# Kernel tuning notes

Measured on AMD Instinct MI355X. Metric: run time of the kernel, lower is better.

The kernel has to match this reference:

```python
import jax, jax.numpy as jnp
import numpy as np

MASK_ID = 3
MAX_SEN = 128
SEN_DIM = 128
EMBED = 1024


def setup_inputs() -> dict:
    key = jax.random.key(0)
    ks = jax.random.split(key, 12)
    B, S, E, D = 8, 8192, EMBED, SEN_DIM
    s = 0.02
    return {
        "input_ids": jax.random.randint(ks[0], (B, S), 0, 64),
        "hidden_states": jax.random.normal(ks[1], (B, S, E), jnp.float32),
        "Wv": jax.random.normal(ks[2], (E, D), jnp.float32) * s,
        "bv": jnp.zeros((D,), jnp.float32),
        "Wq": jax.random.normal(ks[3], (E, D), jnp.float32) * s,
        "bq": jnp.zeros((D,), jnp.float32),
        "Wk": jax.random.normal(ks[4], (D, D), jnp.float32) * s,
        "bk": jnp.zeros((D,), jnp.float32),
        "Wvt": jax.random.normal(ks[5], (D, D), jnp.float32) * s,
        "bvt": jnp.zeros((D,), jnp.float32),
        "Wo": jax.random.normal(ks[6], (D, E), jnp.float32) * s,
        "bo": jnp.zeros((E,), jnp.float32),
    }


def reference(input_ids, hidden_states, Wv, bv, Wq, bq, Wk, bk, Wvt, bvt, Wo, bo):
    B, S, E = hidden_states.shape
    dt = hidden_states.dtype

    # sentence segmentation: each mask token t with running count c belongs to bucket c-1
    mask = input_ids == MASK_ID                               # (B, S)
    csum = jnp.cumsum(mask.astype(jnp.int32), axis=1)         # (B, S)
    # tokens that are not mask tokens (or overflow max_sen_num) go to dummy bucket MAX_SEN
    seg = jnp.where(mask & (csum <= MAX_SEN), csum - 1, MAX_SEN)  # (B, S)

    # segment-sum replacement for torch.bmm(sen_pos_mask, hidden_states)
    b_idx = jnp.arange(B)[:, None]
    pooled = jnp.zeros((B, MAX_SEN + 1, E), dt).at[b_idx, seg].add(hidden_states)[:, :MAX_SEN]  # (B, M, E)

    static_sen_states = pooled @ Wv + bv                      # (B, M, 128)

    q_token = (hidden_states @ Wq + bq) * (SEN_DIM ** -0.5)   # (B, S, 128)
    k_sen = static_sen_states @ Wk + bk                       # (B, M, 128)
    v_sen = static_sen_states @ Wvt + bvt                     # (B, M, 128)

    # token t may attend to sentences 0..csum[t]-1
    tmp_mask = (jnp.arange(MAX_SEN)[None, None, :] + 1) <= csum[:, :, None]  # (B, S, M)
    neg = jnp.finfo(dt).min
    logits = jnp.einsum('bsd,bmd->bsm', q_token, k_sen) + jnp.where(tmp_mask, jnp.zeros((), dt), neg)
    attn = jax.nn.softmax(logits, axis=-1) * tmp_mask.astype(dt)  # (B, S, M)

    sen_attn_output = jnp.einsum('bsm,bmd->bsd', attn, v_sen) @ Wo + bo  # (B, S, E)
    return sen_attn_output
```

## Files before the change

kernel.cpp:

```cpp
#include <hip/hip_runtime.h>
#include <hip/hip_bf16.h>

#define MASK_ID 3
#define MAX_SEN 128
#define NB 8
#define SEQ 8192
#define EMB 1024
#define DIM 128
#define TS 32

typedef __attribute__((ext_vector_type(8))) short short8v;
typedef __attribute__((ext_vector_type(4))) float f32x4;

#define MFMA(a, b, c) __builtin_amdgcn_mfma_f32_16x16x32_bf16(a, b, c, 0, 0, 0)

__device__ __forceinline__ short f2b(float x) {
    union { float f; unsigned u; } v; v.f = x;
    unsigned r = (v.u + 0x7FFFu + ((v.u >> 16) & 1u)) >> 16;
    return (short)r;
}

__global__ __launch_bounds__(1024) void seg_kernel(const int* __restrict__ ids,
                                                   int* __restrict__ pos,
                                                   int* __restrict__ nvis) {
    int b = blockIdx.x;
    int tid = threadIdx.x;
    __shared__ int sc[1024];
    __shared__ int sc2[1024];
    const int PER = SEQ / 1024;
    int base = b * SEQ + tid * PER;

    int ids_l[PER];
    int cnt = 0;
    #pragma unroll
    for (int j = 0; j < PER; j++) {
        ids_l[j] = ids[base + j];
        cnt += (ids_l[j] == MASK_ID) ? 1 : 0;
    }
    if (tid < MAX_SEN) pos[b * MAX_SEN + tid] = -1;
    sc[tid] = cnt;
    __syncthreads();

    int* src = sc;
    int* dst = sc2;
    for (int off = 1; off < 1024; off <<= 1) {
        int v = src[tid];
        if (tid >= off) v += src[tid - off];
        dst[tid] = v;
        __syncthreads();
        int* t = src; src = dst; dst = t;
    }
    int incl = src[tid];
    int run = incl - cnt;

    #pragma unroll
    for (int j = 0; j < PER; j++) {
        if (ids_l[j] == MASK_ID) {
            run++;
            if (run <= MAX_SEN) pos[b * MAX_SEN + run - 1] = tid * PER + j;
        }
        int nv = run; if (nv > MAX_SEN) nv = MAX_SEN;
        nvis[base + j] = nv;
    }
}

__global__ __launch_bounds__(256) void prep_w(const float* __restrict__ Wq,
                                              const float* __restrict__ Wo,
                                              short* __restrict__ WqT,
                                              short* __restrict__ WoT) {
    int idx = blockIdx.x * 256 + threadIdx.x;
    int d = idx >> 10, e = idx & 1023;
    WqT[idx] = f2b(Wq[e * DIM + d]);
    int e2 = idx >> 7, d2 = idx & 127;
    WoT[idx] = f2b(Wo[d2 * EMB + e2]);
}

__global__ __launch_bounds__(128) void static_kernel(const float* __restrict__ hidden,
                                                     const float* __restrict__ Wv,
                                                     const float* __restrict__ bv,
                                                     const int* __restrict__ pos,
                                                     float* __restrict__ stat) {
    int m = blockIdx.x, b = blockIdx.y;
    int d = threadIdx.x;
    __shared__ float h[EMB];
    int p = pos[b * MAX_SEN + m];
    float acc = bv[d];
    if (p >= 0) {
        const float* hp = hidden + ((size_t)b * SEQ + p) * EMB;
        for (int e = d; e < EMB; e += 128) h[e] = hp[e];
        __syncthreads();
        for (int e = 0; e < EMB; e++) acc += h[e] * Wv[e * DIM + d];
    }
    stat[(b * MAX_SEN + m) * DIM + d] = acc;
}

__global__ __launch_bounds__(128) void kv_kernel(const float* __restrict__ stat,
                                                 const float* __restrict__ Wk, const float* __restrict__ bk,
                                                 const float* __restrict__ Wvt, const float* __restrict__ bvt,
                                                 short* __restrict__ k_bf, short* __restrict__ vT_bf) {
    int m = blockIdx.x, b = blockIdx.y;
    int d = threadIdx.x;
    __shared__ float srow[DIM];
    srow[d] = stat[(b * MAX_SEN + m) * DIM + d];
    __syncthreads();
    float ka = bk[d], va = bvt[d];
    for (int e = 0; e < DIM; e++) {
        float sv = srow[e];
        ka += sv * Wk[e * DIM + d];
        va += sv * Wvt[e * DIM + d];
    }
    k_bf[((size_t)b * MAX_SEN + m) * DIM + d] = f2b(ka);
    vT_bf[((size_t)b * DIM + d) * MAX_SEN + m] = f2b(va);
}

__global__ __launch_bounds__(256, 2) void attn_kernel(
    const float* __restrict__ hidden,
    const short* __restrict__ WqT, const float* __restrict__ bq,
    const short* __restrict__ k_bf, const short* __restrict__ vT_bf,
    const short* __restrict__ WoT, const float* __restrict__ bo,
    const int* __restrict__ nvis,
    float* __restrict__ out) {
    int blk = blockIdx.x;
    int b  = blk >> 8;
    int s0 = (blk & 255) * TS;
    int tid = threadIdx.x;
    int lane = tid & 63;
    int w  = tid >> 6;
    int lr = lane & 15;
    int lq = lane >> 4;

    __shared__ short hA[32 * 256];
    __shared__ short qP[32 * 128];
    __shared__ short odB[32 * 128];
    __shared__ float lg[32 * 132];

    char* hAc = (char*)hA;
    char* qPc = (char*)qP;
    char* odc = (char*)odB;

    const size_t hrow = (size_t)b * SEQ + s0;
    f32x4 zero = {0.f, 0.f, 0.f, 0.f};

    f32x4 a00 = zero, a01 = zero, a10 = zero, a11 = zero;
    for (int ec = 0; ec < 4; ec++) {
        __syncthreads();
        #pragma unroll
        for (int g = 0; g < 4; g++) {
            int G = tid + g * 256;
            int t = G >> 5;
            int e8 = (G & 31) << 3;
            const float* hp = hidden + (hrow + t) * EMB + ec * 256 + e8;
            float4 f0 = *(const float4*)hp;
            float4 f1 = *(const float4*)(hp + 4);
            short8v hh;
            hh[0] = f2b(f0.x); hh[1] = f2b(f0.y); hh[2] = f2b(f0.z); hh[3] = f2b(f0.w);
            hh[4] = f2b(f1.x); hh[5] = f2b(f1.y); hh[6] = f2b(f1.z); hh[7] = f2b(f1.w);
            int byte = (t * 512 + e8 * 2) ^ ((t & 7) << 4);
            *(short8v*)(hAc + byte) = hh;
        }
        __syncthreads();
        const short* bp0 = WqT + (w * 32 + lr) * 1024 + ec * 256 + lq * 8;
        const short* bp1 = bp0 + 16 * 1024;
        #pragma unroll
        for (int kk = 0; kk < 8; kk++) {
            short8v fa0 = *(short8v*)(hAc + ((lr * 512 + kk * 64 + lq * 16) ^ ((lr & 7) << 4)));
            short8v fa1 = *(short8v*)(hAc + (((16 + lr) * 512 + kk * 64 + lq * 16) ^ ((lr & 7) << 4)));
            short8v fb0 = *(const short8v*)(bp0 + kk * 32);
            short8v fb1 = *(const short8v*)(bp1 + kk * 32);
            a00 = MFMA(fa0, fb0, a00); a01 = MFMA(fa0, fb1, a01);
            a10 = MFMA(fa1, fb0, a10); a11 = MFMA(fa1, fb1, a11);
        }
    }
    {
        const float scale = 0.08838834764831845f;
        int d0 = w * 32 + lr;
        float bq0 = bq[d0], bq1 = bq[d0 + 16];
        #pragma unroll
        for (int r = 0; r < 4; r++) {
            int r0 = lq * 4 + r, r1 = 16 + r0;
            *(short*)(qPc + ((r0 * 256 + d0 * 2) ^ ((r0 & 7) << 4)))        = f2b((a00[r] + bq0) * scale);
            *(short*)(qPc + ((r0 * 256 + (d0 + 16) * 2) ^ ((r0 & 7) << 4))) = f2b((a01[r] + bq1) * scale);
            *(short*)(qPc + ((r1 * 256 + d0 * 2) ^ ((r1 & 7) << 4)))        = f2b((a10[r] + bq0) * scale);
            *(short*)(qPc + ((r1 * 256 + (d0 + 16) * 2) ^ ((r1 & 7) << 4))) = f2b((a11[r] + bq1) * scale);
        }
    }
    __syncthreads();

    {
        f32x4 l00 = zero, l01 = zero, l10 = zero, l11 = zero;
        const short* kbp0 = k_bf + ((size_t)b << 14) + (w * 32 + lr) * 128 + lq * 8;
        const short* kbp1 = kbp0 + 16 * 128;
        #pragma unroll
        for (int kk = 0; kk < 4; kk++) {
            short8v fa0 = *(short8v*)(qPc + ((lr * 256 + kk * 64 + lq * 16) ^ ((lr & 7) << 4)));
            short8v fa1 = *(short8v*)(qPc + (((16 + lr) * 256 + kk * 64 + lq * 16) ^ ((lr & 7) << 4)));
            short8v fb0 = *(const short8v*)(kbp0 + kk * 32);
            short8v fb1 = *(const short8v*)(kbp1 + kk * 32);
            l00 = MFMA(fa0, fb0, l00); l01 = MFMA(fa0, fb1, l01);
            l10 = MFMA(fa1, fb0, l10); l11 = MFMA(fa1, fb1, l11);
        }
        int m0 = w * 32 + lr;
        #pragma unroll
        for (int r = 0; r < 4; r++) {
            int r0 = lq * 4 + r, r1 = 16 + r0;
            lg[r0 * 132 + m0]      = l00[r];
            lg[r0 * 132 + m0 + 16] = l01[r];
            lg[r1 * 132 + m0]      = l10[r];
            lg[r1 * 132 + m0 + 16] = l11[r];
        }
    }
    __syncthreads();

    {
        int t = tid >> 3, sub = tid & 7;
        int nv = nvis[b * SEQ + s0 + t];
        float pv[16];
        float mx = -3.0e38f;
        #pragma unroll
        for (int i = 0; i < 16; i++) {
            int m = sub * 16 + i;
            float vv = lg[t * 132 + m];
            pv[i] = vv;
            if (m < nv) mx = fmaxf(mx, vv);
        }
        mx = fmaxf(mx, __shfl_xor(mx, 1));
        mx = fmaxf(mx, __shfl_xor(mx, 2));
        mx = fmaxf(mx, __shfl_xor(mx, 4));
        float sum = 0.f;
        #pragma unroll
        for (int i = 0; i < 16; i++) {
            int m = sub * 16 + i;
            float e = (m < nv) ? __expf(pv[i] - mx) : 0.f;
            pv[i] = e;
            sum += e;
        }
        sum += __shfl_xor(sum, 1);
        sum += __shfl_xor(sum, 2);
        sum += __shfl_xor(sum, 4);
        float inv = (nv > 0) ? 1.0f / sum : 0.f;
        #pragma unroll
        for (int i = 0; i < 16; i++) {
            int m = sub * 16 + i;
            *(short*)(qPc + ((t * 256 + m * 2) ^ ((t & 7) << 4))) = f2b(pv[i] * inv);
        }
    }
    __syncthreads();

    {
        f32x4 o00 = zero, o01 = zero, o10 = zero, o11 = zero;
        const short* vbp0 = vT_bf + ((size_t)b << 14) + (w * 32 + lr) * 128 + lq * 8;
        const short* vbp1 = vbp0 + 16 * 128;
        #pragma unroll
        for (int kk = 0; kk < 4; kk++) {
            short8v fa0 = *(short8v*)(qPc + ((lr * 256 + kk * 64 + lq * 16) ^ ((lr & 7) << 4)));
            short8v fa1 = *(short8v*)(qPc + (((16 + lr) * 256 + kk * 64 + lq * 16) ^ ((lr & 7) << 4)));
            short8v fb0 = *(const short8v*)(vbp0 + kk * 32);
            short8v fb1 = *(const short8v*)(vbp1 + kk * 32);
            o00 = MFMA(fa0, fb0, o00); o01 = MFMA(fa0, fb1, o01);
            o10 = MFMA(fa1, fb0, o10); o11 = MFMA(fa1, fb1, o11);
        }
        int d0 = w * 32 + lr;
        #pragma unroll
        for (int r = 0; r < 4; r++) {
            int r0 = lq * 4 + r, r1 = 16 + r0;
            *(short*)(odc + ((r0 * 256 + d0 * 2) ^ ((r0 & 7) << 4)))        = f2b(o00[r]);
            *(short*)(odc + ((r0 * 256 + (d0 + 16) * 2) ^ ((r0 & 7) << 4))) = f2b(o01[r]);
            *(short*)(odc + ((r1 * 256 + d0 * 2) ^ ((r1 & 7) << 4)))        = f2b(o10[r]);
            *(short*)(odc + ((r1 * 256 + (d0 + 16) * 2) ^ ((r1 & 7) << 4))) = f2b(o11[r]);
        }
    }
    __syncthreads();

    {
        short8v af0[4], af1[4];
        #pragma unroll
        for (int kk = 0; kk < 4; kk++) {
            af0[kk] = *(short8v*)(odc + ((lr * 256 + kk * 64 + lq * 16) ^ ((lr & 7) << 4)));
            af1[kk] = *(short8v*)(odc + (((16 + lr) * 256 + kk * 64 + lq * 16) ^ ((lr & 7) << 4)));
        }
        #pragma unroll
        for (int pass = 0; pass < 4; pass++) {
            int ep = w * 256 + pass * 64;
            f32x4 ac0[4], ac1[4];
            #pragma unroll
            for (int e2 = 0; e2 < 4; e2++) { ac0[e2] = zero; ac1[e2] = zero; }
            #pragma unroll
            for (int kk = 0; kk < 4; kk++) {
                #pragma unroll
                for (int e2 = 0; e2 < 4; e2++) {
                    const short8v bb = *(const short8v*)(WoT + (ep + e2 * 16 + lr) * 128 + kk * 32 + lq * 8);
                    ac0[e2] = MFMA(af0[kk], bb, ac0[e2]);
                    ac1[e2] = MFMA(af1[kk], bb, ac1[e2]);
                }
            }
            #pragma unroll
            for (int e2 = 0; e2 < 4; e2++) {
                int col = ep + e2 * 16 + lr;
                float bov = bo[col];
                #pragma unroll
                for (int r = 0; r < 4; r++) {
                    out[(hrow + lq * 4 + r) * EMB + col]      = ac0[e2][r] + bov;
                    out[(hrow + 16 + lq * 4 + r) * EMB + col] = ac1[e2][r] + bov;
                }
            }
        }
    }
}

extern "C" void kernel_launch(void* const* d_in, const int* in_sizes, int n_in,
                              void* d_out, int out_size, void* d_ws, size_t ws_size,
                              hipStream_t stream) {
    const int*   ids    = (const int*)d_in[0];
    const float* hidden = (const float*)d_in[1];
    const float* Wv     = (const float*)d_in[2];
    const float* bv     = (const float*)d_in[3];
    const float* Wq     = (const float*)d_in[4];
    const float* bq     = (const float*)d_in[5];
    const float* Wk     = (const float*)d_in[6];
    const float* bk     = (const float*)d_in[7];
    const float* Wvt    = (const float*)d_in[8];
    const float* bvt    = (const float*)d_in[9];
    const float* Wo     = (const float*)d_in[10];
    const float* bo     = (const float*)d_in[11];

    char* ws = (char*)d_ws;
    int*   pos   = (int*)ws;
    int*   nvis  = (int*)(ws + (4 << 10));
    float* stat  = (float*)(ws + (260 << 10));
    short* k_bf  = (short*)(ws + (772 << 10));
    short* vT_bf = (short*)(ws + (1028 << 10));
    short* WqT   = (short*)(ws + (1284 << 10));
    short* WoT   = (short*)(ws + (1540 << 10));

    seg_kernel<<<NB, 1024, 0, stream>>>(ids, pos, nvis);
    prep_w<<<512, 256, 0, stream>>>(Wq, Wo, WqT, WoT);
    dim3 g2(MAX_SEN, NB);
    static_kernel<<<g2, 128, 0, stream>>>(hidden, Wv, bv, pos, stat);
    kv_kernel<<<g2, 128, 0, stream>>>(stat, Wk, bk, Wvt, bvt, k_bf, vT_bf);
    attn_kernel<<<NB * (SEQ / TS), 256, 0, stream>>>(hidden, WqT, bq, k_bf, vT_bf, WoT, bo,
                                                     nvis, (float*)d_out);
}
```

Measured before the change: 255.4 us.

## Prefetch hidden chunks in registers, alias LDS buffers, fuse static and kv kernels

The attention kernel now loads the next 256-column chunk of hidden states into registers while the current chunk is converted and multiplied. This overlaps global loads with MFMA work. The hidden-chunk LDS buffer and the logits buffer now share one allocation, and launch bounds rise to 4 blocks per CU to raise occupancy. The static-sentence and K/V projection kernels are merged, which removes one launch and the intermediate fp32 buffer. The costs are register pressure from 8 float4 prefetch registers under a tighter register budget, and a possible spill risk.

```diff
diff --git a/kernel.cpp b/kernel.cpp
--- a/kernel.cpp
+++ b/kernel.cpp
@@ -75,14 +75,16 @@
     WoT[idx] = f2b(Wo[d2 * EMB + e2]);
 }
 
-__global__ __launch_bounds__(128) void static_kernel(const float* __restrict__ hidden,
-                                                     const float* __restrict__ Wv,
-                                                     const float* __restrict__ bv,
+__global__ __launch_bounds__(128) void statkv_kernel(const float* __restrict__ hidden,
+                                                     const float* __restrict__ Wv, const float* __restrict__ bv,
+                                                     const float* __restrict__ Wk, const float* __restrict__ bk,
+                                                     const float* __restrict__ Wvt, const float* __restrict__ bvt,
                                                      const int* __restrict__ pos,
-                                                     float* __restrict__ stat) {
+                                                     short* __restrict__ k_bf, short* __restrict__ vT_bf) {
     int m = blockIdx.x, b = blockIdx.y;
     int d = threadIdx.x;
     __shared__ float h[EMB];
+    __shared__ float srow[DIM];
     int p = pos[b * MAX_SEN + m];
     float acc = bv[d];
     if (p >= 0) {
@@ -91,17 +93,7 @@
         __syncthreads();
         for (int e = 0; e < EMB; e++) acc += h[e] * Wv[e * DIM + d];
     }
-    stat[(b * MAX_SEN + m) * DIM + d] = acc;
-}
-
-__global__ __launch_bounds__(128) void kv_kernel(const float* __restrict__ stat,
-                                                 const float* __restrict__ Wk, const float* __restrict__ bk,
-                                                 const float* __restrict__ Wvt, const float* __restrict__ bvt,
-                                                 short* __restrict__ k_bf, short* __restrict__ vT_bf) {
-    int m = blockIdx.x, b = blockIdx.y;
-    int d = threadIdx.x;
-    __shared__ float srow[DIM];
-    srow[d] = stat[(b * MAX_SEN + m) * DIM + d];
+    srow[d] = acc;
     __syncthreads();
     float ka = bk[d], va = bvt[d];
     for (int e = 0; e < DIM; e++) {
@@ -113,7 +105,7 @@
     vT_bf[((size_t)b * DIM + d) * MAX_SEN + m] = f2b(va);
 }
 
-__global__ __launch_bounds__(256, 2) void attn_kernel(
+__global__ __launch_bounds__(256, 4) void attn_kernel(
     const float* __restrict__ hidden,
     const short* __restrict__ WqT, const float* __restrict__ bq,
     const short* __restrict__ k_bf, const short* __restrict__ vT_bf,
@@ -129,17 +121,27 @@
     int lr = lane & 15;
     int lq = lane >> 4;
 
-    __shared__ short hA[32 * 256];
+    __shared__ char uAbuf[32 * 132 * 4];
     __shared__ short qP[32 * 128];
     __shared__ short odB[32 * 128];
-    __shared__ float lg[32 * 132];
-
-    char* hAc = (char*)hA;
+
+    char* hAc = uAbuf;
+    float* lg = (float*)uAbuf;
     char* qPc = (char*)qP;
     char* odc = (char*)odB;
 
     const size_t hrow = (size_t)b * SEQ + s0;
     f32x4 zero = {0.f, 0.f, 0.f, 0.f};
+
+    float4 pf[8];
+    #pragma unroll
+    for (int g = 0; g < 4; g++) {
+        int G = tid + g * 256;
+        int t = G >> 5, e8 = (G & 31) << 3;
+        const float* hp = hidden + (hrow + t) * EMB + e8;
+        pf[2 * g]     = *(const float4*)hp;
+        pf[2 * g + 1] = *(const float4*)(hp + 4);
+    }
 
     f32x4 a00 = zero, a01 = zero, a10 = zero, a11 = zero;
     for (int ec = 0; ec < 4; ec++) {
@@ -147,16 +149,24 @@
         #pragma unroll
         for (int g = 0; g < 4; g++) {
             int G = tid + g * 256;
-            int t = G >> 5;
-            int e8 = (G & 31) << 3;
-            const float* hp = hidden + (hrow + t) * EMB + ec * 256 + e8;
-            float4 f0 = *(const float4*)hp;
-            float4 f1 = *(const float4*)(hp + 4);
+            int t = G >> 5, e8 = (G & 31) << 3;
             short8v hh;
-            hh[0] = f2b(f0.x); hh[1] = f2b(f0.y); hh[2] = f2b(f0.z); hh[3] = f2b(f0.w);
-            hh[4] = f2b(f1.x); hh[5] = f2b(f1.y); hh[6] = f2b(f1.z); hh[7] = f2b(f1.w);
+            hh[0] = f2b(pf[2 * g].x); hh[1] = f2b(pf[2 * g].y);
+            hh[2] = f2b(pf[2 * g].z); hh[3] = f2b(pf[2 * g].w);
+            hh[4] = f2b(pf[2 * g + 1].x); hh[5] = f2b(pf[2 * g + 1].y);
+            hh[6] = f2b(pf[2 * g + 1].z); hh[7] = f2b(pf[2 * g + 1].w);
             int byte = (t * 512 + e8 * 2) ^ ((t & 7) << 4);
             *(short8v*)(hAc + byte) = hh;
+        }
+        if (ec < 3) {
+            #pragma unroll
+            for (int g = 0; g < 4; g++) {
+                int G = tid + g * 256;
+                int t = G >> 5, e8 = (G & 31) << 3;
+                const float* hp = hidden + (hrow + t) * EMB + (ec + 1) * 256 + e8;
+                pf[2 * g]     = *(const float4*)hp;
+                pf[2 * g + 1] = *(const float4*)(hp + 4);
+            }
         }
         __syncthreads();
         const short* bp0 = WqT + (w * 32 + lr) * 1024 + ec * 256 + lq * 8;
@@ -326,17 +336,15 @@
     char* ws = (char*)d_ws;
     int*   pos   = (int*)ws;
     int*   nvis  = (int*)(ws + (4 << 10));
-    float* stat  = (float*)(ws + (260 << 10));
-    short* k_bf  = (short*)(ws + (772 << 10));
-    short* vT_bf = (short*)(ws + (1028 << 10));
-    short* WqT   = (short*)(ws + (1284 << 10));
-    short* WoT   = (short*)(ws + (1540 << 10));
+    short* k_bf  = (short*)(ws + (260 << 10));
+    short* vT_bf = (short*)(ws + (516 << 10));
+    short* WqT   = (short*)(ws + (772 << 10));
+    short* WoT   = (short*)(ws + (1028 << 10));
 
     seg_kernel<<<NB, 1024, 0, stream>>>(ids, pos, nvis);
     prep_w<<<512, 256, 0, stream>>>(Wq, Wo, WqT, WoT);
     dim3 g2(MAX_SEN, NB);
-    static_kernel<<<g2, 128, 0, stream>>>(hidden, Wv, bv, pos, stat);
-    kv_kernel<<<g2, 128, 0, stream>>>(stat, Wk, bk, Wvt, bvt, k_bf, vT_bf);
+    statkv_kernel<<<g2, 128, 0, stream>>>(hidden, Wv, bv, Wk, bk, Wvt, bvt, pos, k_bf, vT_bf);
     attn_kernel<<<NB * (SEQ / TS), 256, 0, stream>>>(hidden, WqT, bq, k_bf, vT_bf, WoT, bo,
                                                      nvis, (float*)d_out);
 }
```

Measured after the change: 243.6 us. 4.6% less time.
